# Kernel tuning notes

Hardware: AMD Instinct MI355X
Metric: run time of the kernel (lower is better)

The kernel has to match this reference:

```python
import jax, jax.numpy as jnp
import numpy as np
from jax import lax

NEG_SLOPE = 0.01
UP = 2
DN = 2
FILTER_LEN = 8

def kaiser_filter(n, fc, beta):
    # Kaiser-windowed sinc lowpass, unit DC gain (standard StyleGAN3-style design)
    t = np.arange(n) - (n - 1) / 2.0
    f = 2.0 * fc * np.sinc(2.0 * fc * t) * np.kaiser(n, beta)
    f = f / f.sum()
    return jnp.asarray(f, dtype=jnp.float32)

def _depthwise_conv1d(x, filt, stride, lhs_dilation, pad_lo, pad_hi):
    # x: [B, C, T]; filt: [K] symmetric taps -> depthwise kernel [C, 1, K]
    C = x.shape[1]
    w = jnp.broadcast_to(filt.reshape(1, 1, -1), (C, 1, filt.shape[0]))
    return lax.conv_general_dilated(
        x, w,
        window_strides=(stride,),
        padding=[(pad_lo, pad_hi)],
        lhs_dilation=(lhs_dilation,),
        dimension_numbers=("NCW", "OIW", "NCW"),
        feature_group_count=C,
    )

def setup_inputs() -> dict:
    key = jax.random.key(0)
    x = jax.random.normal(key, (8, 256, 32768), dtype=jnp.float32)
    up_filter = kaiser_filter(FILTER_LEN * UP + 1, 0.5, 2.5)   # 17 taps
    dn_filter = kaiser_filter(FILTER_LEN * DN + 1, 0.5, 2.5)   # 17 taps
    return {"x": x, "up_filter": up_filter, "dn_filter": dn_filter}

def reference(x, up_filter, dn_filter):
    B, C, T = x.shape
    K = up_filter.shape[0]  # UP*FILTER_LEN + 1
    # conv_transpose1d(stride=UP, padding=p, output_padding=UP-1) ==
    # conv with lhs_dilation=UP and padding (K-1-p, K-1-p+output_padding).
    # Filter is symmetric so kernel flip is a no-op.
    p = UP * FILTER_LEN // 2
    y = _depthwise_conv1d(x, up_filter, stride=1, lhs_dilation=UP,
                          pad_lo=K - 1 - p, pad_hi=K - 1 - p + (UP - 1))
    y = UP * y  # [B, C, UP*T]
    y = jnp.where(y >= 0, y, NEG_SLOPE * y)  # leaky_relu
    pd = DN * FILTER_LEN // 2
    y = _depthwise_conv1d(y, dn_filter, stride=DN, lhs_dilation=1,
                          pad_lo=pd, pad_hi=pd)  # [B, C, T]
    return y
```

## Files before the change

kernel.cpp:

```cpp
#include <hip/hip_runtime.h>
#include <stdint.h>


#define T_LEN 32768
#define R_OUT 8
#define TPR   (T_LEN / R_OUT)

typedef __fp16   cvt2 __attribute__((ext_vector_type(2)));
typedef _Float16 hpair __attribute__((ext_vector_type(2)));

__device__ __forceinline__ uint32_t pkrtz(float lo, float hi) {
    cvt2 p = __builtin_amdgcn_cvt_pkrtz(lo, hi);
    return __builtin_bit_cast(uint32_t, p);
}
__device__ __forceinline__ hpair h2(uint32_t u) {
    return __builtin_bit_cast(hpair, u);
}
__device__ __forceinline__ uint32_t u32(hpair h) {
    return __builtin_bit_cast(uint32_t, h);
}
__device__ __forceinline__ hpair pk_fma(hpair a, hpair b, hpair c) {
    return __builtin_elementwise_fma(a, b, c);
}
__device__ __forceinline__ hpair pk_lrelu(hpair v, hpair c01) {
    return __builtin_elementwise_max(v, v * c01);
}
__device__ __forceinline__ float lrelu(float v) { return fmaxf(v, 0.01f * v); }

__global__ void pack_taps(const float* __restrict__ up,
                          const float* __restrict__ dn,
                          uint32_t* __restrict__ ws) {
    if (threadIdx.x == 0 && blockIdx.x == 0) {
        #pragma unroll
        for (int j = 0; j < 9; ++j) {
            float fe = 2.0f * up[2*j];
            float de = dn[2*j];
            ws[j]      = pkrtz(fe, fe);
            ws[17 + j] = pkrtz(de, de);
        }
        #pragma unroll
        for (int j = 0; j < 8; ++j) {
            float fo = 2.0f * up[2*j+1];
            float dd = dn[2*j+1];
            ws[9 + j]  = pkrtz(fo, fo);
            ws[26 + j] = pkrtz(dd, dd);
        }
    }
}

__global__ void flrelu_pk8t(
    const float* __restrict__ x,
    const float* __restrict__ up,
    const float* __restrict__ dn,
    const uint32_t* __restrict__ tw,
    float* __restrict__ out)
{
    const int gid = blockIdx.x * 256 + threadIdx.x;
    const int row = gid >> 12;
    const int t   = (gid & (TPR - 1)) * R_OUT;
    const float* __restrict__ xrow = x + (size_t)row * T_LEN;
    float* __restrict__ orow       = out + (size_t)row * T_LEN;

    if (t >= 8 && t + R_OUT + 8 <= T_LEN) {
        hpair feB[9], foB[8], deB[9], ddB[8];
        #pragma unroll
        for (int j = 0; j < 9; ++j) { feB[j] = h2(tw[j]); deB[j] = h2(tw[17+j]); }
        #pragma unroll
        for (int j = 0; j < 8; ++j) { foB[j] = h2(tw[9+j]); ddB[j] = h2(tw[26+j]); }
        const hpair c01 = h2(pkrtz(0.01f, 0.01f));

        float xv[24];
        const float4* xp = reinterpret_cast<const float4*>(xrow + t - 8);
        #pragma unroll
        for (int k = 0; k < 6; ++k) {
            float4 v = xp[k];
            xv[4*k+0] = v.x; xv[4*k+1] = v.y;
            xv[4*k+2] = v.z; xv[4*k+3] = v.w;
        }

        uint32_t xau[12], xsu[11];
        #pragma unroll
        for (int k = 0; k < 12; ++k) xau[k] = pkrtz(xv[2*k], xv[2*k+1]);
        #pragma unroll
        for (int k = 0; k < 11; ++k)
            xsu[k] = (xau[k] >> 16) | (xau[k+1] << 16);

        hpair ga[8], goa[8];
        #pragma unroll
        for (int q = 0; q < 8; ++q) {
            hpair s = feB[0] * h2(xau[q]);
            #pragma unroll
            for (int a = 1; a < 5; ++a) s = pk_fma(feB[2*a], h2(xau[q+a]), s);
            #pragma unroll
            for (int a = 0; a < 4; ++a) s = pk_fma(feB[2*a+1], h2(xsu[q+a]), s);
            ga[q] = pk_lrelu(s, c01);

            hpair r = foB[0] * h2(xsu[q]);
            #pragma unroll
            for (int a = 1; a < 4; ++a) r = pk_fma(foB[2*a], h2(xsu[q+a]), r);
            #pragma unroll
            for (int a = 0; a < 4; ++a) r = pk_fma(foB[2*a+1], h2(xau[q+a+1]), r);
            goa[q] = pk_lrelu(r, c01);
        }

        hpair gs[7], gos[7];
        #pragma unroll
        for (int q = 0; q < 7; ++q) {
            gs[q]  = h2((u32(ga[q])  >> 16) | (u32(ga[q+1])  << 16));
            gos[q] = h2((u32(goa[q]) >> 16) | (u32(goa[q+1]) << 16));
        }

        hpair zp[4];
        #pragma unroll
        for (int p = 0; p < 4; ++p) {
            hpair s = deB[0] * ga[p];
            #pragma unroll
            for (int a = 1; a < 5; ++a) s = pk_fma(deB[2*a], ga[p+a], s);
            #pragma unroll
            for (int a = 0; a < 4; ++a) s = pk_fma(deB[2*a+1], gs[p+a], s);
            #pragma unroll
            for (int a = 0; a < 4; ++a) s = pk_fma(ddB[2*a], goa[p+a], s);
            #pragma unroll
            for (int a = 0; a < 4; ++a) s = pk_fma(ddB[2*a+1], gos[p+a], s);
            zp[p] = s;
        }

        float4* op = reinterpret_cast<float4*>(orow + t);
        #pragma unroll
        for (int k = 0; k < 2; ++k)
            op[k] = make_float4((float)zp[2*k][0], (float)zp[2*k][1],
                                (float)zp[2*k+1][0], (float)zp[2*k+1][1]);
    } else {
        float fe[9], fo[8], de[9], dd[8];
        #pragma unroll
        for (int j = 0; j < 9; ++j) { fe[j] = 2.0f * up[2*j]; de[j] = dn[2*j]; }
        #pragma unroll
        for (int j = 0; j < 8; ++j) { fo[j] = 2.0f * up[2*j+1]; dd[j] = dn[2*j+1]; }

        float xv[R_OUT + 16];
        #pragma unroll
        for (int i = 0; i < R_OUT + 16; ++i) {
            int g = t - 8 + i;
            xv[i] = (g >= 0 && g < T_LEN) ? xrow[g] : 0.0f;
        }
        float acc[R_OUT];
        #pragma unroll
        for (int r = 0; r < R_OUT; ++r) acc[r] = 0.0f;

        #pragma unroll
        for (int ml = 0; ml < R_OUT + 8; ++ml) {
            float ae = 0.0f;
            #pragma unroll
            for (int j = 0; j < 9; ++j) ae = fmaf(fe[j], xv[ml+j], ae);
            float g = lrelu(ae);
            int m = t - 4 + ml;
            if (m < 0 || m >= T_LEN) g = 0.0f;
            #pragma unroll
            for (int r = 0; r < R_OUT; ++r)
                if (r >= ml - 8 && r <= ml)
                    acc[r] = fmaf(de[ml-r], g, acc[r]);

            if (ml < R_OUT + 7) {
                float ao = 0.0f;
                #pragma unroll
                for (int j = 0; j < 8; ++j) ao = fmaf(fo[j], xv[ml+1+j], ao);
                float h = lrelu(ao);
                if (m < 0 || m >= T_LEN) h = 0.0f;
                #pragma unroll
                for (int r = 0; r < R_OUT; ++r)
                    if (r >= ml - 7 && r <= ml)
                        acc[r] = fmaf(dd[ml-r], h, acc[r]);
            }
        }

        float4* op = reinterpret_cast<float4*>(orow + t);
        #pragma unroll
        for (int k = 0; k < R_OUT / 4; ++k)
            op[k] = make_float4(acc[4*k+0], acc[4*k+1], acc[4*k+2], acc[4*k+3]);
    }
}

extern "C" void kernel_launch(void* const* d_in, const int* in_sizes, int n_in,
                              void* d_out, int out_size, void* d_ws, size_t ws_size,
                              hipStream_t stream) {
    const float* x  = (const float*)d_in[0];
    const float* up = (const float*)d_in[1];
    const float* dn = (const float*)d_in[2];
    float* out      = (float*)d_out;
    uint32_t* ws    = (uint32_t*)d_ws;

    pack_taps<<<1, 64, 0, stream>>>(up, dn, ws);

    const int rows    = in_sizes[0] / T_LEN;
    const int threads = rows * TPR;
    flrelu_pk8t<<<threads / 256, 256, 0, stream>>>(x, up, dn, ws, out);
}
```

Measured before the change: 118.7 us.

## Share upsampled intermediate through LDS to eliminate per-thread halo recompute

Each thread now computes only its own 8 upsampled/leaky-relu pairs (instead of 16 with overlapping halo) and writes them to shared memory. After a block barrier, each thread reads its neighbours' values for the downsampling filter. Four extra threads compute the block-end halo. This roughly halves the upsample FMA work and reduces the x loads per thread, at the cost of LDS traffic, a __syncthreads, and a more serial tail for the halo threads.

```diff
diff --git a/kernel.cpp b/kernel.cpp
--- a/kernel.cpp
+++ b/kernel.cpp
@@ -4,7 +4,11 @@
 
 #define T_LEN 32768
 #define R_OUT 8
-#define TPR   (T_LEN / R_OUT)
+#define BLK   256
+#define OUTB  (BLK * R_OUT)
+#define BPR   (T_LEN / OUTB)
+#define HPAIR (OUTB / 2)
+#define NPAIR (HPAIR + 4)
 
 typedef __fp16   cvt2 __attribute__((ext_vector_type(2)));
 typedef _Float16 hpair __attribute__((ext_vector_type(2)));
@@ -48,135 +52,158 @@
     }
 }
 
-__global__ void flrelu_pk8t(
+__global__ __launch_bounds__(256) void flrelu_lds(
     const float* __restrict__ x,
     const float* __restrict__ up,
     const float* __restrict__ dn,
     const uint32_t* __restrict__ tw,
     float* __restrict__ out)
 {
-    const int gid = blockIdx.x * 256 + threadIdx.x;
-    const int row = gid >> 12;
-    const int t   = (gid & (TPR - 1)) * R_OUT;
+    __shared__ uint32_t sga[NPAIR];
+    __shared__ uint32_t sgo[NPAIR];
+
+    const int tid = threadIdx.x;
+    const int row = blockIdx.x >> 4;
+    const int blk = blockIdx.x & (BPR - 1);
+    const int t0  = blk * OUTB;
+    const int t   = t0 + tid * R_OUT;
     const float* __restrict__ xrow = x + (size_t)row * T_LEN;
     float* __restrict__ orow       = out + (size_t)row * T_LEN;
 
-    if (t >= 8 && t + R_OUT + 8 <= T_LEN) {
-        hpair feB[9], foB[8], deB[9], ddB[8];
-        #pragma unroll
-        for (int j = 0; j < 9; ++j) { feB[j] = h2(tw[j]); deB[j] = h2(tw[17+j]); }
-        #pragma unroll
-        for (int j = 0; j < 8; ++j) { foB[j] = h2(tw[9+j]); ddB[j] = h2(tw[26+j]); }
-        const hpair c01 = h2(pkrtz(0.01f, 0.01f));
-
-        float xv[24];
-        const float4* xp = reinterpret_cast<const float4*>(xrow + t - 8);
-        #pragma unroll
-        for (int k = 0; k < 6; ++k) {
-            float4 v = xp[k];
-            xv[4*k+0] = v.x; xv[4*k+1] = v.y;
-            xv[4*k+2] = v.z; xv[4*k+3] = v.w;
-        }
-
-        uint32_t xau[12], xsu[11];
-        #pragma unroll
-        for (int k = 0; k < 12; ++k) xau[k] = pkrtz(xv[2*k], xv[2*k+1]);
-        #pragma unroll
-        for (int k = 0; k < 11; ++k)
+    hpair feB[9], foB[8], deB[9], ddB[8];
+    #pragma unroll
+    for (int j = 0; j < 9; ++j) { feB[j] = h2(tw[j]); deB[j] = h2(tw[17+j]); }
+    #pragma unroll
+    for (int j = 0; j < 8; ++j) { foB[j] = h2(tw[9+j]); ddB[j] = h2(tw[26+j]); }
+    const hpair c01 = h2(pkrtz(0.01f, 0.01f));
+
+    const bool safe = (blk == 0) || (blk == BPR - 1);
+
+    {
+        float xv[16];
+        if (!safe) {
+            const float4* xp = reinterpret_cast<const float4*>(xrow + t - 8);
+            #pragma unroll
+            for (int k = 0; k < 4; ++k) {
+                float4 v = xp[k];
+                xv[4*k+0] = v.x; xv[4*k+1] = v.y;
+                xv[4*k+2] = v.z; xv[4*k+3] = v.w;
+            }
+        } else {
+            #pragma unroll
+            for (int i = 0; i < 16; ++i) {
+                int g = t - 8 + i;
+                xv[i] = (g >= 0 && g < T_LEN) ? xrow[g] : 0.0f;
+            }
+        }
+
+        uint32_t xau[8], xsu[7];
+        #pragma unroll
+        for (int k = 0; k < 8; ++k) xau[k] = pkrtz(xv[2*k], xv[2*k+1]);
+        #pragma unroll
+        for (int k = 0; k < 7; ++k)
             xsu[k] = (xau[k] >> 16) | (xau[k+1] << 16);
 
-        hpair ga[8], goa[8];
-        #pragma unroll
-        for (int q = 0; q < 8; ++q) {
+        uint32_t ga[4], go[4];
+        #pragma unroll
+        for (int q = 0; q < 4; ++q) {
             hpair s = feB[0] * h2(xau[q]);
             #pragma unroll
             for (int a = 1; a < 5; ++a) s = pk_fma(feB[2*a], h2(xau[q+a]), s);
             #pragma unroll
             for (int a = 0; a < 4; ++a) s = pk_fma(feB[2*a+1], h2(xsu[q+a]), s);
-            ga[q] = pk_lrelu(s, c01);
+            ga[q] = u32(pk_lrelu(s, c01));
 
             hpair r = foB[0] * h2(xsu[q]);
             #pragma unroll
             for (int a = 1; a < 4; ++a) r = pk_fma(foB[2*a], h2(xsu[q+a]), r);
             #pragma unroll
             for (int a = 0; a < 4; ++a) r = pk_fma(foB[2*a+1], h2(xau[q+a+1]), r);
-            goa[q] = pk_lrelu(r, c01);
-        }
-
-        hpair gs[7], gos[7];
-        #pragma unroll
-        for (int q = 0; q < 7; ++q) {
-            gs[q]  = h2((u32(ga[q])  >> 16) | (u32(ga[q+1])  << 16));
-            gos[q] = h2((u32(goa[q]) >> 16) | (u32(goa[q+1]) << 16));
+            go[q] = u32(pk_lrelu(r, c01));
+        }
+
+        if (safe) {
+            #pragma unroll
+            for (int q = 0; q < 4; ++q) {
+                int m0 = t - 4 + 2*q;
+                uint32_t msk = ((m0 >= 0 && m0 < T_LEN) ? 0x0000FFFFu : 0u)
+                             | ((m0+1 >= 0 && m0+1 < T_LEN) ? 0xFFFF0000u : 0u);
+                ga[q] &= msk; go[q] &= msk;
+            }
+        }
+
+        *reinterpret_cast<uint4*>(&sga[4*tid]) =
+            make_uint4(ga[0], ga[1], ga[2], ga[3]);
+        *reinterpret_cast<uint4*>(&sgo[4*tid]) =
+            make_uint4(go[0], go[1], go[2], go[3]);
+    }
+
+    if (tid < 4) {
+        float fe[9], fo[8];
+        #pragma unroll
+        for (int j = 0; j < 9; ++j) fe[j] = 2.0f * up[2*j];
+        #pragma unroll
+        for (int j = 0; j < 8; ++j) fo[j] = 2.0f * up[2*j+1];
+
+        const int p  = HPAIR + tid;
+        const int m0 = t0 - 4 + 2*p;
+        float xw[10];
+        #pragma unroll
+        for (int i = 0; i < 10; ++i) {
+            int g = m0 - 4 + i;
+            xw[i] = (g >= 0 && g < T_LEN) ? xrow[g] : 0.0f;
+        }
+        float g0 = 0.f, g1 = 0.f, h0 = 0.f, h1 = 0.f;
+        #pragma unroll
+        for (int j = 0; j < 9; ++j) { g0 = fmaf(fe[j], xw[j], g0);
+                                      g1 = fmaf(fe[j], xw[j+1], g1); }
+        #pragma unroll
+        for (int j = 0; j < 8; ++j) { h0 = fmaf(fo[j], xw[j+1], h0);
+                                      h1 = fmaf(fo[j], xw[j+2], h1); }
+        g0 = lrelu(g0); g1 = lrelu(g1); h0 = lrelu(h0); h1 = lrelu(h1);
+        if (!(m0   >= 0 && m0   < T_LEN)) { g0 = 0.f; h0 = 0.f; }
+        if (!(m0+1 >= 0 && m0+1 < T_LEN)) { g1 = 0.f; h1 = 0.f; }
+        sga[p] = pkrtz(g0, g1);
+        sgo[p] = pkrtz(h0, h1);
+    }
+
+    __syncthreads();
+
+    {
+        uint4 A0 = *reinterpret_cast<const uint4*>(&sga[4*tid]);
+        uint4 A1 = *reinterpret_cast<const uint4*>(&sga[4*tid + 4]);
+        uint4 B0 = *reinterpret_cast<const uint4*>(&sgo[4*tid]);
+        uint4 B1 = *reinterpret_cast<const uint4*>(&sgo[4*tid + 4]);
+        uint32_t gaF[8] = {A0.x, A0.y, A0.z, A0.w, A1.x, A1.y, A1.z, A1.w};
+        uint32_t goF[8] = {B0.x, B0.y, B0.z, B0.w, B1.x, B1.y, B1.z, B1.w};
+
+        uint32_t gs[7], gos[7];
+        #pragma unroll
+        for (int k = 0; k < 7; ++k) {
+            gs[k]  = (gaF[k] >> 16) | (gaF[k+1] << 16);
+            gos[k] = (goF[k] >> 16) | (goF[k+1] << 16);
         }
 
         hpair zp[4];
         #pragma unroll
         for (int p = 0; p < 4; ++p) {
-            hpair s = deB[0] * ga[p];
-            #pragma unroll
-            for (int a = 1; a < 5; ++a) s = pk_fma(deB[2*a], ga[p+a], s);
-            #pragma unroll
-            for (int a = 0; a < 4; ++a) s = pk_fma(deB[2*a+1], gs[p+a], s);
-            #pragma unroll
-            for (int a = 0; a < 4; ++a) s = pk_fma(ddB[2*a], goa[p+a], s);
-            #pragma unroll
-            for (int a = 0; a < 4; ++a) s = pk_fma(ddB[2*a+1], gos[p+a], s);
+            hpair s = deB[0] * h2(gaF[p]);
+            #pragma unroll
+            for (int a = 1; a < 5; ++a) s = pk_fma(deB[2*a], h2(gaF[p+a]), s);
+            #pragma unroll
+            for (int a = 0; a < 4; ++a) s = pk_fma(deB[2*a+1], h2(gs[p+a]), s);
+            #pragma unroll
+            for (int a = 0; a < 4; ++a) s = pk_fma(ddB[2*a], h2(goF[p+a]), s);
+            #pragma unroll
+            for (int a = 0; a < 4; ++a) s = pk_fma(ddB[2*a+1], h2(gos[p+a]), s);
             zp[p] = s;
         }
 
         float4* op = reinterpret_cast<float4*>(orow + t);
-        #pragma unroll
-        for (int k = 0; k < 2; ++k)
-            op[k] = make_float4((float)zp[2*k][0], (float)zp[2*k][1],
-                                (float)zp[2*k+1][0], (float)zp[2*k+1][1]);
-    } else {
-        float fe[9], fo[8], de[9], dd[8];
-        #pragma unroll
-        for (int j = 0; j < 9; ++j) { fe[j] = 2.0f * up[2*j]; de[j] = dn[2*j]; }
-        #pragma unroll
-        for (int j = 0; j < 8; ++j) { fo[j] = 2.0f * up[2*j+1]; dd[j] = dn[2*j+1]; }
-
-        float xv[R_OUT + 16];
-        #pragma unroll
-        for (int i = 0; i < R_OUT + 16; ++i) {
-            int g = t - 8 + i;
-            xv[i] = (g >= 0 && g < T_LEN) ? xrow[g] : 0.0f;
-        }
-        float acc[R_OUT];
-        #pragma unroll
-        for (int r = 0; r < R_OUT; ++r) acc[r] = 0.0f;
-
-        #pragma unroll
-        for (int ml = 0; ml < R_OUT + 8; ++ml) {
-            float ae = 0.0f;
-            #pragma unroll
-            for (int j = 0; j < 9; ++j) ae = fmaf(fe[j], xv[ml+j], ae);
-            float g = lrelu(ae);
-            int m = t - 4 + ml;
-            if (m < 0 || m >= T_LEN) g = 0.0f;
-            #pragma unroll
-            for (int r = 0; r < R_OUT; ++r)
-                if (r >= ml - 8 && r <= ml)
-                    acc[r] = fmaf(de[ml-r], g, acc[r]);
-
-            if (ml < R_OUT + 7) {
-                float ao = 0.0f;
-                #pragma unroll
-                for (int j = 0; j < 8; ++j) ao = fmaf(fo[j], xv[ml+1+j], ao);
-                float h = lrelu(ao);
-                if (m < 0 || m >= T_LEN) h = 0.0f;
-                #pragma unroll
-                for (int r = 0; r < R_OUT; ++r)
-                    if (r >= ml - 7 && r <= ml)
-                        acc[r] = fmaf(dd[ml-r], h, acc[r]);
-            }
-        }
-
-        float4* op = reinterpret_cast<float4*>(orow + t);
-        #pragma unroll
-        for (int k = 0; k < R_OUT / 4; ++k)
-            op[k] = make_float4(acc[4*k+0], acc[4*k+1], acc[4*k+2], acc[4*k+3]);
+        op[0] = make_float4((float)zp[0][0], (float)zp[0][1],
+                            (float)zp[1][0], (float)zp[1][1]);
+        op[1] = make_float4((float)zp[2][0], (float)zp[2][1],
+                            (float)zp[3][0], (float)zp[3][1]);
     }
 }
 
@@ -191,7 +218,7 @@
 
     pack_taps<<<1, 64, 0, stream>>>(up, dn, ws);
 
-    const int rows    = in_sizes[0] / T_LEN;
-    const int threads = rows * TPR;
-    flrelu_pk8t<<<threads / 256, 256, 0, stream>>>(x, up, dn, ws, out);
-}
+    const int rows   = in_sizes[0] / T_LEN;
+    const int blocks = rows * BPR;
+    flrelu_lds<<<blocks, BLK, 0, stream>>>(x, up, dn, ws, out);
+}
```

Result: slower. 262.6 us (+121.3%).
